# Performance work log

Measured on AMD Instinct MI355X. Metric: run time of the kernel, lower is better.

Reference implementation:

```python
import jax, jax.numpy as jnp
import numpy as np

N = 100000   # nodes
E = 1600000  # edges
D_IN, D_H, D_OUT = 128, 256, 128
EPS = 1e-5


def _linear_params(key, fan_in, fan_out):
    lim = 1.0 / np.sqrt(fan_in)
    kw, kb = jax.random.split(key)
    W = jax.random.uniform(kw, (fan_in, fan_out), minval=-lim, maxval=lim, dtype=jnp.float32)
    b = jax.random.uniform(kb, (fan_out,), minval=-lim, maxval=lim, dtype=jnp.float32)
    return W, b


def setup_inputs() -> dict:
    key = jax.random.key(0)
    ks = jax.random.split(key, 8)
    W1, b1 = _linear_params(ks[0], D_IN, D_H)
    W2, b2 = _linear_params(ks[1], D_H, D_H)
    W3, b3 = _linear_params(ks[2], D_H, D_OUT)
    return {
        'feat': jax.random.normal(ks[3], (N, D_IN), dtype=jnp.float32),
        'W1': W1, 'b1': b1, 'g1': jnp.ones(D_H, jnp.float32), 'be1': jnp.zeros(D_H, jnp.float32), 'a1': jnp.full((1,), 0.25, jnp.float32),
        'W2': W2, 'b2': b2, 'g2': jnp.ones(D_H, jnp.float32), 'be2': jnp.zeros(D_H, jnp.float32), 'a2': jnp.full((1,), 0.25, jnp.float32),
        'W3': W3, 'b3': b3,
        'src': jax.random.randint(ks[4], (E,), 0, N, dtype=jnp.int32),
        'dst': jax.random.randint(ks[5], (E,), 0, N, dtype=jnp.int32),
    }


def _layer_norm(x, g, b):
    mu = jnp.mean(x, axis=-1, keepdims=True)
    var = jnp.mean((x - mu) ** 2, axis=-1, keepdims=True)
    return g * (x - mu) / jnp.sqrt(var + EPS) + b


def _prelu(x, a):
    return jnp.where(x >= 0, x, a * x)


def reference(feat, W1, b1, g1, be1, a1, W2, b2, g2, be2, a2, W3, b3, src, dst):
    ones = jnp.ones((E,), jnp.float32)
    # out-degree (of src nodes) and in-degree (of dst nodes), clamped to >= 1
    deg_out = jnp.maximum(jax.ops.segment_sum(ones, src, num_segments=N), 1.0) ** -0.5  # [N]
    deg_in = jnp.maximum(jax.ops.segment_sum(ones, dst, num_segments=N), 1.0) ** -0.5   # [N]

    def conv(h, W, b, g=None, be=None, a=None):
        x = h * deg_out[:, None]                                   # src-side degree norm
        agg = jax.ops.segment_sum(x[src], dst, num_segments=N)     # sparse sum aggregation
        r = (agg @ W + b) * deg_in[:, None]                        # linear + dst-side norm
        if g is not None:
            r = _prelu(_layer_norm(r, g, be), a)
        return r

    h = conv(feat, W1, b1, g1, be1, a1)
    h = conv(h, W2, b2, g2, be2, a2)
    h = conv(h, W3, b3)  # last layer: encoding=False -> no norm, no activation
    return h
```

## Files before the change

kernel.cpp:

```cpp
#include <hip/hip_runtime.h>
#include <cstdint>
#include <cstddef>

static constexpr int NN = 100000;
static constexpr int NE = 1600000;
static constexpr int NP = 100096;

static constexpr int NBUCK  = 391;
static constexpr int BCAP   = 5120;
static constexpr int NBUCKD = 782;
static constexpr int BCAPD  = 2816;
static constexpr int SCAP   = 128;
static constexpr int PBLK   = 200;
static constexpr int EPB    = 8000;

typedef __attribute__((ext_vector_type(8))) short short8;
typedef __attribute__((ext_vector_type(8))) unsigned short ushort8;
typedef __attribute__((ext_vector_type(4))) unsigned short ushort4v;
typedef __attribute__((ext_vector_type(4))) float f32x4;

__device__ inline ushort bf16_rtn(float x) {
    uint32_t u = __float_as_uint(x);
    uint32_t r = u + 0x7fffu + ((u >> 16) & 1u);
    return (ushort)(r >> 16);
}
__device__ inline float bf16_to_f(ushort u) {
    return __uint_as_float((uint32_t)u << 16);
}

__global__ __launch_bounds__(256) void k_init_cur(int* __restrict__ curA) {
    int b = blockIdx.x * 256 + threadIdx.x;
    if (b < NBUCK) curA[b] = b * BCAP;
}

__global__ __launch_bounds__(256) void k_partA(const int* __restrict__ src, const int* __restrict__ dst,
                                               int* __restrict__ curA, int* __restrict__ pairA) {
    __shared__ int hs[NBUCK];
    int e0 = blockIdx.x * EPB;
    for (int i = threadIdx.x; i < NBUCK; i += 256) hs[i] = 0;
    __syncthreads();
    for (int e = e0 + (int)threadIdx.x; e < e0 + EPB; e += 256)
        atomicAdd(&hs[src[e] >> 8], 1);
    __syncthreads();
    for (int i = threadIdx.x; i < NBUCK; i += 256) {
        int c = hs[i];
        hs[i] = c ? atomicAdd(&curA[i], c) : 0;
    }
    __syncthreads();
    for (int e = e0 + (int)threadIdx.x; e < e0 + EPB; e += 256) {
        int s = src[e], d = dst[e];
        int p = atomicAdd(&hs[s >> 8], 1);
        pairA[p] = (d << 8) | (s & 255);
    }
}

__global__ __launch_bounds__(256) void k_degout(const int* __restrict__ curA, const int* __restrict__ pairA,
                                                float* __restrict__ deg_out_inv) {
    __shared__ int h[256];
    int b = blockIdx.x;
    int p0 = b * BCAP;
    int n = curA[b] - p0;
    h[threadIdx.x] = 0;
    __syncthreads();
    for (int i = threadIdx.x; i < n; i += 256)
        atomicAdd(&h[pairA[p0 + i] & 255], 1);
    __syncthreads();
    int node = b * 256 + (int)threadIdx.x;
    if (node < NN)
        deg_out_inv[node] = rsqrtf(fmaxf((float)h[threadIdx.x], 1.0f));
}

__global__ __launch_bounds__(256) void k_countB(const int* __restrict__ curA, const int* __restrict__ pairA,
                                                int* __restrict__ cntB) {
    __shared__ int h[NBUCKD];
    int s = blockIdx.x;
    int p0 = s * BCAP;
    int n = curA[s] - p0;
    for (int i = threadIdx.x; i < NBUCKD; i += 256) h[i] = 0;
    __syncthreads();
    for (int i = threadIdx.x; i < n; i += 256)
        atomicAdd(&h[pairA[p0 + i] >> 15], 1);
    __syncthreads();
    for (int i = threadIdx.x; i < NBUCKD; i += 256)
        cntB[s * NBUCKD + i] = h[i];
}

__global__ __launch_bounds__(512) void k_scanB(const int* __restrict__ cntB, int* __restrict__ offB,
                                               int* __restrict__ fillB) {
    __shared__ int sd[512];
    int b = blockIdx.x;
    int t = threadIdx.x;
    int v = (t < NBUCK) ? cntB[t * NBUCKD + b] : 0;
    sd[t] = v;
    __syncthreads();
    #pragma unroll
    for (int off = 1; off < 512; off <<= 1) {
        int x = (t >= off) ? sd[t - off] : 0;
        __syncthreads();
        sd[t] += x;
        __syncthreads();
    }
    if (t < NBUCK) offB[t * NBUCKD + b] = b * BCAPD + sd[t] - v;
    if (t == NBUCK - 1) fillB[b] = sd[t];
}

__global__ __launch_bounds__(256) void k_placeB(const int* __restrict__ curA, const int* __restrict__ pairA,
                                                const int* __restrict__ offB, int* __restrict__ pairB) {
    __shared__ int cur[NBUCKD];
    int s = blockIdx.x;
    int p0 = s * BCAP;
    int n = curA[s] - p0;
    for (int i = threadIdx.x; i < NBUCKD; i += 256) cur[i] = offB[s * NBUCKD + i];
    __syncthreads();
    int sbase = s << 8;
    for (int i = threadIdx.x; i < n; i += 256) {
        int pk = pairA[p0 + i];
        int d = pk >> 8;
        int sfull = sbase | (pk & 255);
        int pos = atomicAdd(&cur[d >> 7], 1);
        pairB[pos] = (sfull << 7) | (d & 127);
    }
}

__global__ __launch_bounds__(256) void k_deg_in(const int* __restrict__ fillB, const int* __restrict__ pairB,
                                                float* __restrict__ deg_in_inv) {
    __shared__ int h[128];
    int b = blockIdx.x;
    int p0 = b * BCAPD;
    int n = fillB[b];
    if (threadIdx.x < 128) h[threadIdx.x] = 0;
    __syncthreads();
    for (int i = threadIdx.x; i < n; i += 256)
        atomicAdd(&h[pairB[p0 + i] & 127], 1);
    __syncthreads();
    if (threadIdx.x < 128) {
        int node = b * 128 + (int)threadIdx.x;
        deg_in_inv[node] = rsqrtf(fmaxf((float)h[threadIdx.x], 1.0f));
    }
}

__global__ __launch_bounds__(512) void k_split32(const int* __restrict__ fillB, const int* __restrict__ pairB,
                                                 int* __restrict__ pairB2, int* __restrict__ fillS) {
    __shared__ int se[BCAPD];
    int b = blockIdx.x;
    int n = fillB[b];
    const int* ep = pairB + (size_t)b * BCAPD;
    for (int i = threadIdx.x; i < n; i += 512) se[i] = ep[i];
    __syncthreads();
    int w = threadIdx.x >> 6;
    int l = threadIdx.x & 63;
    for (int r = 0; r < 4; ++r) {
        int h = w + 8 * r;
        int* op = pairB2 + (size_t)(b * 32 + h) * SCAP;
        int cnt = 0;
        for (int i0 = 0; i0 < n; i0 += 64) {
            int idx = i0 + l;
            int pk = (idx < n) ? se[idx] : 0;
            bool match = (idx < n) && ((pk & 31) == h);
            unsigned long long mask = __ballot(match);
            if (match) {
                int pos = __popcll(mask & ((1ull << l) - 1ull));
                op[cnt + pos] = pk;
            }
            cnt += __popcll(mask);
        }
        if (l == 0) fillS[b * 32 + h] = cnt;
    }
}

__global__ __launch_bounds__(256) void k_cvt(const float* __restrict__ feat,
                                             const float* __restrict__ deg_out_inv,
                                             ushort* __restrict__ out) {
    int idx = blockIdx.x * 256 + threadIdx.x;
    if (idx >= NN * 32) return;
    float4 v = *(const float4*)(feat + (size_t)idx * 4);
    float w = deg_out_inv[idx >> 5];
    ushort4 o;
    o.x = bf16_rtn(v.x * w);
    o.y = bf16_rtn(v.y * w);
    o.z = bf16_rtn(v.z * w);
    o.w = bf16_rtn(v.w * w);
    *(ushort4*)(out + (size_t)idx * 4) = o;
}

template <int XSTRIDE, int COLOFF, bool FINAL>
__global__ __launch_bounds__(1024) void k_agg_push5(const int* __restrict__ pairB2,
                                                    const int* __restrict__ fillS,
                                                    const ushort* __restrict__ x,
                                                    const float* __restrict__ bias,
                                                    const float* __restrict__ deg_in_inv,
                                                    ushort* __restrict__ out_b, float* __restrict__ out_f) {
    int b = blockIdx.x;
    int h = (int)threadIdx.x >> 5;
    int l5 = (int)threadIdx.x & 31;
    int sb = b * 32 + h;
    int m = fillS[sb];
    const int* ep = pairB2 + (size_t)sb * SCAP;
    const ushort* xb = x + COLOFF + l5 * 4;
    f32x4 acc[4];
    #pragma unroll
    for (int r = 0; r < 4; ++r) acc[r] = (f32x4){0.f, 0.f, 0.f, 0.f};
    for (int i = 0; i < m; i += 2) {
        int pk0 = ep[i];
        int i1 = (i + 1 < m) ? (i + 1) : i;
        int pk1 = ep[i1];
        float wt1 = (i + 1 < m) ? 1.0f : 0.0f;
        ushort4v v0 = *(const ushort4v*)(xb + (size_t)(pk0 >> 7) * XSTRIDE);
        ushort4v v1 = *(const ushort4v*)(xb + (size_t)(pk1 >> 7) * XSTRIDE);
        int s0 = (pk0 >> 5) & 3;
        int s1 = (pk1 >> 5) & 3;
        #pragma unroll
        for (int r = 0; r < 4; ++r) {
            float w0 = (s0 == r) ? 1.0f : 0.0f;
            float w1 = (s1 == r) ? wt1 : 0.0f;
            #pragma unroll
            for (int k = 0; k < 4; ++k)
                acc[r][k] = fmaf(w0, bf16_to_f(v0[k]),
                             fmaf(w1, bf16_to_f(v1[k]), acc[r][k]));
        }
    }
    if constexpr (FINAL) {
        float4 bv = *(const float4*)(bias + COLOFF + l5 * 4);
        #pragma unroll
        for (int r = 0; r < 4; ++r) {
            int node = b * 128 + h + 32 * r;
            if (node < NN) {
                float dv = deg_in_inv[node];
                float4 o;
                o.x = (acc[r][0] + bv.x) * dv;
                o.y = (acc[r][1] + bv.y) * dv;
                o.z = (acc[r][2] + bv.z) * dv;
                o.w = (acc[r][3] + bv.w) * dv;
                *(float4*)(out_f + (size_t)node * 128 + COLOFF + l5 * 4) = o;
            }
        }
    } else {
        #pragma unroll
        for (int r = 0; r < 4; ++r) {
            int node = b * 128 + h + 32 * r;
            ushort4v u;
            #pragma unroll
            for (int k = 0; k < 4; ++k) u[k] = bf16_rtn(acc[r][k]);
            *(ushort4v*)(out_b + (size_t)node * XSTRIDE + COLOFF + l5 * 4) = u;
        }
    }
}

template <int K, int M>
__device__ inline void packW_dev(const float* __restrict__ W, ushort* __restrict__ out, int blk) {
    constexpr int NT = M / 16, KC = K / 32;
    constexpr int WTOT = KC * NT * 512;
    int idx = blk * 256 + (int)threadIdx.x;
    int lane = idx & 63;
    int tile = idx >> 6;
    int nt = tile % NT, kc = tile / NT;
    int col = nt * 16 + (lane & 15);
    int kbase = kc * 32 + (lane >> 4) * 8;
    size_t o = (size_t)tile * 512 + lane * 8;
    #pragma unroll
    for (int j = 0; j < 8; ++j) {
        float w = W[(size_t)(kbase + j) * M + col];
        uint32_t u = __float_as_uint(w);
        uint32_t hu = u & 0xffff0000u;
        float lf = w - __uint_as_float(hu);
        out[o + j] = (ushort)(u >> 16);
        out[o + WTOT + j] = (ushort)(__float_as_uint(lf) >> 16);
    }
}

__global__ __launch_bounds__(256) void k_packAll(const float* __restrict__ W1, ushort* __restrict__ o1,
                                                 const float* __restrict__ W2, ushort* __restrict__ o2,
                                                 const float* __restrict__ W3, ushort* __restrict__ o3) {
    int b = blockIdx.x;
    if (b < 16) packW_dev<128, 256>(W1, o1, b);
    else if (b < 48) packW_dev<256, 256>(W2, o2, b - 16);
    else packW_dev<256, 128>(W3, o3, b - 48);
}

template <int K, int M, int MODE>
__global__ __launch_bounds__(256) void k_gemm_mfma(const ushort* __restrict__ A,
                                                   const ushort* __restrict__ Wp,
                                                   const float* __restrict__ bias,
                                                   const float* __restrict__ deg_in_inv,
                                                   const float* __restrict__ deg_out_inv,
                                                   const float* __restrict__ g,
                                                   const float* __restrict__ be,
                                                   const float* __restrict__ a,
                                                   ushort* __restrict__ out) {
    constexpr int NT = M / 16;
    constexpr int KC = K / 32;
    constexpr int WTOT = KC * NT * 512;
    constexpr int COLW = M / 64;
    constexpr int ROWW = 4 / COLW;
    constexpr int BROWS = 64 * ROWW;
    constexpr int LROW = M + 8;
    constexpr int NRF = BROWS / 16;
    constexpr int RFW = NRF / 4;
    __shared__ ushort sbuf[BROWS * LROW];
    __shared__ float sredS[4][64];
    __shared__ float sredQ[4][64];
    __shared__ float smu[64];
    __shared__ float srs[64];
    static_assert(BROWS * LROW >= 2 * NRF * 512, "staging dbuf must fit in sbuf");

    int lane = threadIdx.x & 63;
    int wave = threadIdx.x >> 6;
    int cw = wave % COLW;
    int rw = wave / COLW;
    int m = lane & 15;
    int quad = lane >> 4;
    int rowb = blockIdx.x * BROWS + rw * 64;

    f32x4 acc[4][4];
    #pragma unroll
    for (int rf = 0; rf < 4; ++rf)
        #pragma unroll
        for (int ct = 0; ct < 4; ++ct) acc[rf][ct] = (f32x4){0.f, 0.f, 0.f, 0.f};

    const size_t arow0 = (size_t)blockIdx.x * BROWS;
    auto stage = [&](int kc, int buf) {
        #pragma unroll
        for (int s = 0; s < RFW; ++s) {
            int rf = wave * RFW + s;
            const ushort* gsrc = A + (arow0 + rf * 16 + m) * K + kc * 32 + quad * 8;
            ushort* ldst = sbuf + (size_t)(buf * NRF + rf) * 512;
            __builtin_amdgcn_global_load_lds(
                (const __attribute__((address_space(1))) unsigned int*)gsrc,
                (__attribute__((address_space(3))) unsigned int*)ldst, 16, 0, 0);
        }
    };
    stage(0, 0);
    __syncthreads();
    for (int kc = 0; kc < KC; ++kc) {
        if (kc + 1 < KC) stage(kc + 1, (kc + 1) & 1);
        const ushort* ab = sbuf + (size_t)((kc & 1) * NRF + rw * 4) * 512 + lane * 8;
        short8 av[4];
        #pragma unroll
        for (int rf = 0; rf < 4; ++rf)
            av[rf] = *(const short8*)(ab + rf * 512);
        const ushort* wb0 = Wp + ((size_t)kc * NT + cw * 4) * 512 + lane * 8;
        #pragma unroll
        for (int ct = 0; ct < 4; ++ct) {
            short8 bh = *(const short8*)(wb0 + ct * 512);
            short8 bl = *(const short8*)(wb0 + WTOT + ct * 512);
            #pragma unroll
            for (int rf = 0; rf < 4; ++rf) {
                acc[rf][ct] = __builtin_amdgcn_mfma_f32_16x16x32_bf16(av[rf], bh, acc[rf][ct], 0, 0, 0);
                acc[rf][ct] = __builtin_amdgcn_mfma_f32_16x16x32_bf16(av[rf], bl, acc[rf][ct], 0, 0, 0);
            }
        }
        __syncthreads();
    }
    if constexpr (MODE == 1) {
        float bia[4];
        #pragma unroll
        for (int ct = 0; ct < 4; ++ct) bia[ct] = bias[cw * 64 + ct * 16 + m];
        float din[4][4], fold[4][4];
        #pragma unroll
        for (int rf = 0; rf < 4; ++rf)
            #pragma unroll
            for (int r = 0; r < 4; ++r) {
                int row = rowb + rf * 16 + quad * 4 + r;
                din[rf][r] = deg_in_inv[row];
                fold[rf][r] = deg_out_inv[row];
            }
        float s[4][4], q[4][4];
        #pragma unroll
        for (int rf = 0; rf < 4; ++rf)
            #pragma unroll
            for (int r = 0; r < 4; ++r) { s[rf][r] = 0.f; q[rf][r] = 0.f; }
        #pragma unroll
        for (int rf = 0; rf < 4; ++rf)
            #pragma unroll
            for (int ct = 0; ct < 4; ++ct)
                #pragma unroll
                for (int r = 0; r < 4; ++r) {
                    float v = (acc[rf][ct][r] + bia[ct]) * din[rf][r];
                    acc[rf][ct][r] = v;
                    s[rf][r] += v;
                    q[rf][r] += v * v;
                }
        #pragma unroll
        for (int w = 1; w < 16; w <<= 1)
            #pragma unroll
            for (int rf = 0; rf < 4; ++rf)
                #pragma unroll
                for (int r = 0; r < 4; ++r) {
                    s[rf][r] += __shfl_xor(s[rf][r], w);
                    q[rf][r] += __shfl_xor(q[rf][r], w);
                }
        if (m == 0) {
            #pragma unroll
            for (int rf = 0; rf < 4; ++rf)
                #pragma unroll
                for (int r = 0; r < 4; ++r) {
                    int rl = rf * 16 + quad * 4 + r;
                    sredS[wave][rl] = s[rf][r];
                    sredQ[wave][rl] = q[rf][r];
                }
        }
        __syncthreads();
        if (threadIdx.x < 64) {
            int rl = threadIdx.x;
            float st = sredS[0][rl] + sredS[1][rl] + sredS[2][rl] + sredS[3][rl];
            float qt = sredQ[0][rl] + sredQ[1][rl] + sredQ[2][rl] + sredQ[3][rl];
            float mu = st * (1.0f / M);
            float var = qt * (1.0f / M) - mu * mu;
            smu[rl] = mu;
            srs[rl] = rsqrtf(var + 1e-5f);
        }
        __syncthreads();
        float alpha = a[0];
        float gv[4], bev[4];
        #pragma unroll
        for (int ct = 0; ct < 4; ++ct) {
            gv[ct] = g[cw * 64 + ct * 16 + m];
            bev[ct] = be[cw * 64 + ct * 16 + m];
        }
        #pragma unroll
        for (int rf = 0; rf < 4; ++rf)
            #pragma unroll
            for (int r = 0; r < 4; ++r) {
                int rl = rf * 16 + quad * 4 + r;
                float mu = smu[rl];
                float rs = srs[rl];
                float fo = fold[rf][r];
                #pragma unroll
                for (int ct = 0; ct < 4; ++ct) {
                    float v = gv[ct] * (acc[rf][ct][r] - mu) * rs + bev[ct];
                    v = (v >= 0.0f) ? v : alpha * v;
                    v *= fo;
                    sbuf[rl * LROW + cw * 64 + ct * 16 + m] = bf16_rtn(v);
                }
            }
    } else {
        #pragma unroll
        for (int rf = 0; rf < 4; ++rf)
            #pragma unroll
            for (int ct = 0; ct < 4; ++ct)
                #pragma unroll
                for (int r = 0; r < 4; ++r)
                    sbuf[(rw * 64 + rf * 16 + quad * 4 + r) * LROW + cw * 64 + ct * 16 + m] =
                        bf16_rtn(acc[rf][ct][r]);
    }
    __syncthreads();
    constexpr int CNT = BROWS * M / 256;
    int trow = ((int)threadIdx.x * CNT) / M;
    int tcol = ((int)threadIdx.x * CNT) % M;
    const ushort* rsrc = sbuf + trow * LROW + tcol;
    ushort* gdst = out + (size_t)(blockIdx.x * BROWS + trow) * M + tcol;
    #pragma unroll
    for (int j = 0; j < CNT / 8; ++j) {
        ushort8 v = *(const ushort8*)(rsrc + j * 8);
        *(ushort8*)(gdst + j * 8) = v;
    }
}

extern "C" void kernel_launch(void* const* d_in, const int* in_sizes, int n_in,
                              void* d_out, int out_size, void* d_ws, size_t ws_size,
                              hipStream_t stream) {
    const float* feat = (const float*)d_in[0];
    const float* W1 = (const float*)d_in[1];
    const float* b1 = (const float*)d_in[2];
    const float* g1 = (const float*)d_in[3];
    const float* be1 = (const float*)d_in[4];
    const float* a1 = (const float*)d_in[5];
    const float* W2 = (const float*)d_in[6];
    const float* b2 = (const float*)d_in[7];
    const float* g2 = (const float*)d_in[8];
    const float* be2 = (const float*)d_in[9];
    const float* a2 = (const float*)d_in[10];
    const float* W3 = (const float*)d_in[11];
    const float* b3 = (const float*)d_in[12];
    const int* src = (const int*)d_in[13];
    const int* dst = (const int*)d_in[14];

    char* ws = (char*)d_ws;
    size_t off = 0;
    auto alloc = [&](size_t bytes) -> void* {
        off = (off + 511) & ~(size_t)511;
        void* p = ws + off;
        off += bytes;
        return p;
    };
    int* curA = (int*)alloc((size_t)NBUCK * 4);
    float* deg_out_inv = (float*)alloc((size_t)NP * 4);
    float* deg_in_inv = (float*)alloc((size_t)NP * 4);
    int* pairA = (int*)alloc((size_t)NBUCK * BCAP * 4);
    int* pairB = (int*)alloc((size_t)NBUCKD * BCAPD * 4);
    int* pairB2 = (int*)alloc((size_t)NBUCKD * 32 * SCAP * 4);
    int* fillS = (int*)alloc((size_t)NBUCKD * 32 * 4);
    int* cntB = (int*)alloc((size_t)NBUCK * NBUCKD * 4);
    int* offB = (int*)alloc((size_t)NBUCK * NBUCKD * 4);
    int* fillB = (int*)alloc((size_t)NBUCKD * 4);
    ushort* Wp1 = (ushort*)alloc((size_t)2 * 4 * 16 * 512 * 2);
    ushort* Wp2 = (ushort*)alloc((size_t)2 * 8 * 16 * 512 * 2);
    ushort* Wp3 = (ushort*)alloc((size_t)2 * 8 * 8 * 512 * 2);
    ushort* featb = (ushort*)alloc((size_t)NP * 128 * 2);
    ushort* aggb  = (ushort*)alloc((size_t)NP * 256 * 2);
    ushort* hb    = (ushort*)alloc((size_t)NP * 256 * 2);
    ushort* yb    = (ushort*)alloc((size_t)NP * 128 * 2);
    (void)ws_size; (void)in_sizes; (void)n_in; (void)out_size;

    k_init_cur<<<2, 256, 0, stream>>>(curA);
    k_partA<<<PBLK, 256, 0, stream>>>(src, dst, curA, pairA);
    k_degout<<<NBUCK, 256, 0, stream>>>(curA, pairA, deg_out_inv);
    k_countB<<<NBUCK, 256, 0, stream>>>(curA, pairA, cntB);
    k_scanB<<<NBUCKD, 512, 0, stream>>>(cntB, offB, fillB);
    k_placeB<<<NBUCK, 256, 0, stream>>>(curA, pairA, offB, pairB);
    k_deg_in<<<NBUCKD, 256, 0, stream>>>(fillB, pairB, deg_in_inv);
    k_split32<<<NBUCKD, 512, 0, stream>>>(fillB, pairB, pairB2, fillS);

    k_packAll<<<64, 256, 0, stream>>>(W1, Wp1, W2, Wp2, W3, Wp3);
    k_cvt<<<(NN * 32 + 255) / 256, 256, 0, stream>>>(feat, deg_out_inv, featb);

    k_agg_push5<128, 0, false><<<NBUCKD, 1024, 0, stream>>>(pairB2, fillS, featb, nullptr, nullptr, aggb, nullptr);
    k_gemm_mfma<128, 256, 1><<<NP / 64, 256, 0, stream>>>(aggb, Wp1, b1, deg_in_inv, deg_out_inv, g1, be1, a1, hb);

    k_agg_push5<256, 0, false><<<NBUCKD, 1024, 0, stream>>>(pairB2, fillS, hb, nullptr, nullptr, aggb, nullptr);
    k_agg_push5<256, 128, false><<<NBUCKD, 1024, 0, stream>>>(pairB2, fillS, hb, nullptr, nullptr, aggb, nullptr);
    k_gemm_mfma<256, 256, 1><<<NP / 64, 256, 0, stream>>>(aggb, Wp2, b2, deg_in_inv, deg_out_inv, g2, be2, a2, hb);

    k_gemm_mfma<256, 128, 0><<<NP / 128, 256, 0, stream>>>(hb, Wp3, nullptr, nullptr, nullptr, nullptr, nullptr, nullptr, yb);
    k_agg_push5<128, 0, true><<<NBUCKD, 1024, 0, stream>>>(pairB2, fillS, yb, b3, deg_in_inv, nullptr, (float*)d_out);
}
```

Before: 707.9 us.

## Sort edges by destination slot and aggregate 256-wide features in one pass

The split kernel now groups each 32-row sub-bucket's edges by their exact destination slot (4 segments), stores plain source indices and per-slot counts. The aggregation kernel then walks each segment with plain adds instead of masked FMAs into four accumulators, cutting ALU work per edge. For the 256-wide layer it loads 8 bf16 per lane and covers all columns in one launch, replacing two 128-column passes that each re-read the edge lists. The split kernel now scans the shared edge list four times as often, and the aggregation kernel holds more accumulator registers at D=256.

```diff
diff --git a/kernel.cpp b/kernel.cpp
--- a/kernel.cpp
+++ b/kernel.cpp
@@ -139,8 +139,8 @@
     }
 }
 
-__global__ __launch_bounds__(512) void k_split32(const int* __restrict__ fillB, const int* __restrict__ pairB,
-                                                 int* __restrict__ pairB2, int* __restrict__ fillS) {
+__global__ __launch_bounds__(512) void k_split32s(const int* __restrict__ fillB, const int* __restrict__ pairB,
+                                                  int* __restrict__ esrc2, int* __restrict__ fillS4) {
     __shared__ int se[BCAPD];
     int b = blockIdx.x;
     int n = fillB[b];
@@ -149,22 +149,26 @@
     __syncthreads();
     int w = threadIdx.x >> 6;
     int l = threadIdx.x & 63;
-    for (int r = 0; r < 4; ++r) {
-        int h = w + 8 * r;
-        int* op = pairB2 + (size_t)(b * 32 + h) * SCAP;
+    for (int r4 = 0; r4 < 4; ++r4) {
+        int h = w + 8 * r4;
+        int* op = esrc2 + (size_t)(b * 32 + h) * SCAP;
         int cnt = 0;
-        for (int i0 = 0; i0 < n; i0 += 64) {
-            int idx = i0 + l;
-            int pk = (idx < n) ? se[idx] : 0;
-            bool match = (idx < n) && ((pk & 31) == h);
-            unsigned long long mask = __ballot(match);
-            if (match) {
-                int pos = __popcll(mask & ((1ull << l) - 1ull));
-                op[cnt + pos] = pk;
-            }
-            cnt += __popcll(mask);
-        }
-        if (l == 0) fillS[b * 32 + h] = cnt;
+        for (int slot = 0; slot < 4; ++slot) {
+            int target = h + 32 * slot;
+            int segStart = cnt;
+            for (int i0 = 0; i0 < n; i0 += 64) {
+                int idx = i0 + l;
+                int pk = (idx < n) ? se[idx] : 0;
+                bool match = (idx < n) && ((pk & 127) == target);
+                unsigned long long mask = __ballot(match);
+                if (match) {
+                    int pos = __popcll(mask & ((1ull << l) - 1ull));
+                    op[cnt + pos] = pk >> 7;
+                }
+                cnt += __popcll(mask);
+            }
+            if (l == 0) fillS4[(b * 32 + h) * 4 + slot] = cnt - segStart;
+        }
     }
 }
 
@@ -183,67 +187,99 @@
     *(ushort4*)(out + (size_t)idx * 4) = o;
 }
 
-template <int XSTRIDE, int COLOFF, bool FINAL>
-__global__ __launch_bounds__(1024) void k_agg_push5(const int* __restrict__ pairB2,
-                                                    const int* __restrict__ fillS,
+template <int D, bool FINAL>
+__global__ __launch_bounds__(1024) void k_agg_push6(const int* __restrict__ esrc2,
+                                                    const int* __restrict__ fillS4,
                                                     const ushort* __restrict__ x,
                                                     const float* __restrict__ bias,
                                                     const float* __restrict__ deg_in_inv,
                                                     ushort* __restrict__ out_b, float* __restrict__ out_f) {
+    constexpr int VEC = D / 32;
+    constexpr int NC = VEC / 4;
     int b = blockIdx.x;
     int h = (int)threadIdx.x >> 5;
     int l5 = (int)threadIdx.x & 31;
     int sb = b * 32 + h;
-    int m = fillS[sb];
-    const int* ep = pairB2 + (size_t)sb * SCAP;
-    const ushort* xb = x + COLOFF + l5 * 4;
-    f32x4 acc[4];
+    const int* ep = esrc2 + (size_t)sb * SCAP;
+    int4 cnts = *(const int4*)(fillS4 + (size_t)sb * 4);
+    const ushort* xb = x + l5 * VEC;
+    f32x4 a0[NC], a1[NC], a2[NC], a3[NC];
     #pragma unroll
-    for (int r = 0; r < 4; ++r) acc[r] = (f32x4){0.f, 0.f, 0.f, 0.f};
-    for (int i = 0; i < m; i += 2) {
-        int pk0 = ep[i];
-        int i1 = (i + 1 < m) ? (i + 1) : i;
-        int pk1 = ep[i1];
-        float wt1 = (i + 1 < m) ? 1.0f : 0.0f;
-        ushort4v v0 = *(const ushort4v*)(xb + (size_t)(pk0 >> 7) * XSTRIDE);
-        ushort4v v1 = *(const ushort4v*)(xb + (size_t)(pk1 >> 7) * XSTRIDE);
-        int s0 = (pk0 >> 5) & 3;
-        int s1 = (pk1 >> 5) & 3;
-        #pragma unroll
-        for (int r = 0; r < 4; ++r) {
-            float w0 = (s0 == r) ? 1.0f : 0.0f;
-            float w1 = (s1 == r) ? wt1 : 0.0f;
-            #pragma unroll
-            for (int k = 0; k < 4; ++k)
-                acc[r][k] = fmaf(w0, bf16_to_f(v0[k]),
-                             fmaf(w1, bf16_to_f(v1[k]), acc[r][k]));
-        }
-    }
-    if constexpr (FINAL) {
-        float4 bv = *(const float4*)(bias + COLOFF + l5 * 4);
-        #pragma unroll
-        for (int r = 0; r < 4; ++r) {
-            int node = b * 128 + h + 32 * r;
+    for (int c = 0; c < NC; ++c) {
+        a0[c] = (f32x4){0.f, 0.f, 0.f, 0.f};
+        a1[c] = (f32x4){0.f, 0.f, 0.f, 0.f};
+        a2[c] = (f32x4){0.f, 0.f, 0.f, 0.f};
+        a3[c] = (f32x4){0.f, 0.f, 0.f, 0.f};
+    }
+    int base = 0;
+    auto seg = [&](f32x4 (&A)[NC], int cnt) {
+        int i = 0;
+        for (; i + 2 <= cnt; i += 2) {
+            int s0 = ep[base + i];
+            int s1 = ep[base + i + 1];
+            if constexpr (VEC == 4) {
+                ushort4v v0 = *(const ushort4v*)(xb + (size_t)s0 * D);
+                ushort4v v1 = *(const ushort4v*)(xb + (size_t)s1 * D);
+                #pragma unroll
+                for (int k = 0; k < 4; ++k)
+                    A[0][k] += bf16_to_f(v0[k]) + bf16_to_f(v1[k]);
+            } else {
+                ushort8 v0 = *(const ushort8*)(xb + (size_t)s0 * D);
+                ushort8 v1 = *(const ushort8*)(xb + (size_t)s1 * D);
+                #pragma unroll
+                for (int k = 0; k < 8; ++k)
+                    A[k >> 2][k & 3] += bf16_to_f(v0[k]) + bf16_to_f(v1[k]);
+            }
+        }
+        if (i < cnt) {
+            int s0 = ep[base + i];
+            if constexpr (VEC == 4) {
+                ushort4v v0 = *(const ushort4v*)(xb + (size_t)s0 * D);
+                #pragma unroll
+                for (int k = 0; k < 4; ++k) A[0][k] += bf16_to_f(v0[k]);
+            } else {
+                ushort8 v0 = *(const ushort8*)(xb + (size_t)s0 * D);
+                #pragma unroll
+                for (int k = 0; k < 8; ++k) A[k >> 2][k & 3] += bf16_to_f(v0[k]);
+            }
+        }
+        base += cnt;
+    };
+    seg(a0, cnts.x);
+    seg(a1, cnts.y);
+    seg(a2, cnts.z);
+    seg(a3, cnts.w);
+    auto wb = [&](f32x4 (&A)[NC], int r) {
+        int node = b * 128 + h + 32 * r;
+        if constexpr (FINAL) {
             if (node < NN) {
                 float dv = deg_in_inv[node];
+                float4 bv = *(const float4*)(bias + l5 * 4);
                 float4 o;
-                o.x = (acc[r][0] + bv.x) * dv;
-                o.y = (acc[r][1] + bv.y) * dv;
-                o.z = (acc[r][2] + bv.z) * dv;
-                o.w = (acc[r][3] + bv.w) * dv;
-                *(float4*)(out_f + (size_t)node * 128 + COLOFF + l5 * 4) = o;
-            }
-        }
-    } else {
-        #pragma unroll
-        for (int r = 0; r < 4; ++r) {
-            int node = b * 128 + h + 32 * r;
-            ushort4v u;
-            #pragma unroll
-            for (int k = 0; k < 4; ++k) u[k] = bf16_rtn(acc[r][k]);
-            *(ushort4v*)(out_b + (size_t)node * XSTRIDE + COLOFF + l5 * 4) = u;
-        }
-    }
+                o.x = (A[0][0] + bv.x) * dv;
+                o.y = (A[0][1] + bv.y) * dv;
+                o.z = (A[0][2] + bv.z) * dv;
+                o.w = (A[0][3] + bv.w) * dv;
+                *(float4*)(out_f + (size_t)node * 128 + l5 * 4) = o;
+            }
+        } else {
+            if constexpr (VEC == 4) {
+                ushort4v u;
+                #pragma unroll
+                for (int k = 0; k < 4; ++k) u[k] = bf16_rtn(A[0][k]);
+                *(ushort4v*)(out_b + (size_t)node * D + l5 * 4) = u;
+            } else {
+                ushort8 u;
+                #pragma unroll
+                for (int k = 0; k < 8; ++k) u[k] = bf16_rtn(A[k >> 2][k & 3]);
+                *(ushort8*)(out_b + (size_t)node * D + l5 * 8) = u;
+            }
+        }
+    };
+    wb(a0, 0);
+    wb(a1, 1);
+    wb(a2, 2);
+    wb(a3, 3);
 }
 
 template <int K, int M>
@@ -488,8 +524,8 @@
     float* deg_in_inv = (float*)alloc((size_t)NP * 4);
     int* pairA = (int*)alloc((size_t)NBUCK * BCAP * 4);
     int* pairB = (int*)alloc((size_t)NBUCKD * BCAPD * 4);
-    int* pairB2 = (int*)alloc((size_t)NBUCKD * 32 * SCAP * 4);
-    int* fillS = (int*)alloc((size_t)NBUCKD * 32 * 4);
+    int* esrc2 = (int*)alloc((size_t)NBUCKD * 32 * SCAP * 4);
+    int* fillS4 = (int*)alloc((size_t)NBUCKD * 32 * 4 * 4);
     int* cntB = (int*)alloc((size_t)NBUCK * NBUCKD * 4);
     int* offB = (int*)alloc((size_t)NBUCK * NBUCKD * 4);
     int* fillB = (int*)alloc((size_t)NBUCKD * 4);
@@ -509,18 +545,17 @@
     k_scanB<<<NBUCKD, 512, 0, stream>>>(cntB, offB, fillB);
     k_placeB<<<NBUCK, 256, 0, stream>>>(curA, pairA, offB, pairB);
     k_deg_in<<<NBUCKD, 256, 0, stream>>>(fillB, pairB, deg_in_inv);
-    k_split32<<<NBUCKD, 512, 0, stream>>>(fillB, pairB, pairB2, fillS);
+    k_split32s<<<NBUCKD, 512, 0, stream>>>(fillB, pairB, esrc2, fillS4);
 
     k_packAll<<<64, 256, 0, stream>>>(W1, Wp1, W2, Wp2, W3, Wp3);
     k_cvt<<<(NN * 32 + 255) / 256, 256, 0, stream>>>(feat, deg_out_inv, featb);
 
-    k_agg_push5<128, 0, false><<<NBUCKD, 1024, 0, stream>>>(pairB2, fillS, featb, nullptr, nullptr, aggb, nullptr);
+    k_agg_push6<128, false><<<NBUCKD, 1024, 0, stream>>>(esrc2, fillS4, featb, nullptr, nullptr, aggb, nullptr);
     k_gemm_mfma<128, 256, 1><<<NP / 64, 256, 0, stream>>>(aggb, Wp1, b1, deg_in_inv, deg_out_inv, g1, be1, a1, hb);
 
-    k_agg_push5<256, 0, false><<<NBUCKD, 1024, 0, stream>>>(pairB2, fillS, hb, nullptr, nullptr, aggb, nullptr);
-    k_agg_push5<256, 128, false><<<NBUCKD, 1024, 0, stream>>>(pairB2, fillS, hb, nullptr, nullptr, aggb, nullptr);
+    k_agg_push6<256, false><<<NBUCKD, 1024, 0, stream>>>(esrc2, fillS4, hb, nullptr, nullptr, aggb, nullptr);
     k_gemm_mfma<256, 256, 1><<<NP / 64, 256, 0, stream>>>(aggb, Wp2, b2, deg_in_inv, deg_out_inv, g2, be2, a2, hb);
 
     k_gemm_mfma<256, 128, 0><<<NP / 128, 256, 0, stream>>>(hb, Wp3, nullptr, nullptr, nullptr, nullptr, nullptr, nullptr, yb);
-    k_agg_push5<128, 0, true><<<NBUCKD, 1024, 0, stream>>>(pairB2, fillS, yb, b3, deg_in_inv, nullptr, (float*)d_out);
-}
+    k_agg_push6<128, true><<<NBUCKD, 1024, 0, stream>>>(esrc2, fillS4, yb, b3, deg_in_inv, nullptr, (float*)d_out);
+}
```

Measured after the change: 731.4 us. 3.3% more time.
